# Performance work log

Hardware: AMD Instinct MI355X
Metric: run time of the kernel (lower is better)

Reference implementation:

```python
import jax, jax.numpy as jnp
import numpy as np

LAYERS = 16; SUBLAYERS = 12; NPLANES = LAYERS * SUBLAYERS
POS_LEVEL = 10; DEPTH_LEVEL = 8; ORDER = 3; BASIS_OUT = 8
HIDDEN = 384; BASIS_HIDDEN = 64
SLOPE = 0.01; SIG_OFF = 5.0
IN_H = 512; IN_W = 768; RAYS = 1024
OFFSET = 0.0


def leaky(x):
    return jnp.where(x >= 0, x, SLOPE * x)


def grid_sample_3d(vol, gx, gy, gz):
    # vol (C, D, H, W); grid coords normalized [-1,1]; align_corners=True, zeros padding
    C, Dm, H, W = vol.shape
    x = (gx + 1.0) * 0.5 * (W - 1)
    y = (gy + 1.0) * 0.5 * (H - 1)
    z = (gz + 1.0) * 0.5 * (Dm - 1)
    x0 = jnp.floor(x); y0 = jnp.floor(y); z0 = jnp.floor(z)
    flat = vol.reshape(C, -1)
    out = jnp.zeros((C,) + x.shape, vol.dtype)
    for dz in (0.0, 1.0):
        for dy in (0.0, 1.0):
            for dx in (0.0, 1.0):
                xi = x0 + dx; yi = y0 + dy; zi = z0 + dz
                w = (1 - jnp.abs(x - xi)) * (1 - jnp.abs(y - yi)) * (1 - jnp.abs(z - zi))
                valid = ((xi >= 0) & (xi < W) & (yi >= 0) & (yi < H) & (zi >= 0) & (zi < Dm)).astype(vol.dtype)
                idx = ((jnp.clip(zi, 0, Dm - 1) * H + jnp.clip(yi, 0, H - 1)) * W
                       + jnp.clip(xi, 0, W - 1)).astype(jnp.int32)
                out = out + (w * valid)[None] * jnp.take(flat, idx, axis=1)
    return out


def _rotation(angle, axis):
    axis = np.asarray(axis, np.float64); axis /= np.linalg.norm(axis)
    K = np.array([[0, -axis[2], axis[1]], [axis[2], 0, -axis[0]], [-axis[1], axis[0], 0]])
    R = np.eye(3) + np.sin(angle) * K + (1 - np.cos(angle)) * (K @ K)
    return jnp.asarray(R, jnp.float32)


def setup_inputs() -> dict:
    key = jax.random.key(0)
    ks = jax.random.split(key, 32)
    def lin(i, fan_in, fan_out):
        w = jax.random.normal(ks[i], (fan_in, fan_out), jnp.float32) / np.sqrt(fan_in).astype(np.float32)
        b = jnp.zeros((fan_out,), jnp.float32)
        return w, b
    in_dim = 2 * (2 * POS_LEVEL + DEPTH_LEVEL)     # 56
    out_dim = 1 + BASIS_OUT * 3                    # 25
    w0, b0 = lin(0, in_dim, HIDDEN)
    w1, b1 = lin(1, HIDDEN, HIDDEN)
    w2, b2 = lin(2, HIDDEN, HIDDEN)
    w3, b3 = lin(3, HIDDEN, HIDDEN)
    w4, b4 = lin(4, HIDDEN, HIDDEN)
    wo, bo = lin(5, HIDDEN, out_dim)
    bw0, bb0 = lin(6, 4 * ORDER, BASIS_HIDDEN)
    bw1, bb1 = lin(7, BASIS_HIDDEN, BASIS_HIDDEN)
    bwo, bbo = lin(8, BASIS_HIDDEN, BASIS_OUT)
    mpi_c = jax.random.uniform(ks[20], (LAYERS, 3, IN_H, IN_W), jnp.float32, -1.0, 1.0)
    K = jnp.array([[600.0, 0.0, IN_W / 2.0], [0.0, 600.0, IN_H / 2.0], [0.0, 0.0, 1.0]], jnp.float32)
    planes = jnp.asarray(1.0 / np.linspace(1.0, 0.1, NPLANES), jnp.float32)  # inverse-depth spacing, dmin=1 dmax=10
    selection = jax.random.randint(ks[21], (RAYS,), 0, IN_H * IN_W)
    return dict(
        mpi_c=mpi_c, w0=w0, b0=b0, w1=w1, b1=b1, w2=w2, b2=b2, w3=w3, b3=b3, w4=w4, b4=b4,
        wo=wo, bo=bo, bw0=bw0, bb0=bb0, bw1=bw1, bb1=bb1, bwo=bwo, bbo=bbo,
        ref_rT=jnp.eye(3, dtype=jnp.float32), ref_t=jnp.zeros((3, 1), jnp.float32), ref_k=K,
        feat_r=_rotation(0.03, [0.2, 1.0, 0.1]),
        feat_t=jnp.array([[0.08], [0.03], [0.02]], jnp.float32),
        feat_center=jnp.array([[-0.08], [-0.03], [-0.02]], jnp.float32),
        feat_k=K, planes=planes, selection=selection, out_h=IN_H, out_w=IN_W)


def reference(mpi_c, w0, b0, w1, b1, w2, b2, w3, b3, w4, b4, wo, bo,
              bw0, bb0, bw1, bb1, bwo, bbo,
              ref_rT, ref_t, ref_k, feat_r, feat_t, feat_center, feat_k,
              planes, selection, out_h, out_w):
    # ---- homography warp (computeHomographies / computeHomoWarp) ----
    ki = jnp.linalg.inv(feat_k)
    new_r = feat_r @ ref_rT
    new_t = -new_r @ ref_t + feat_t
    nvec = jnp.array([[0.0, 0.0, 1.0]], jnp.float32)
    Ha = new_r.T
    Hb = Ha @ new_t @ nvec @ Ha
    Hc = (nvec @ Ha @ new_t)[0, 0]
    Hs = ref_k @ (Ha + Hb / (-planes[:, None, None] - Hc)) @ ki      # (P,3,3)
    coords = jnp.stack([(selection % out_w).astype(jnp.float32),
                        (selection // out_w).astype(jnp.float32),
                        jnp.ones_like(selection, jnp.float32)], -1)   # (R,3)
    prod = jnp.einsum('rc,pkc->prk', coords, Hs)                      # (P,R,3)
    ref_coords = prod[..., :2] / prod[..., 2:]                        # (P,R,2)
    scale = jnp.array([IN_W - 1.0, IN_H - 1.0], jnp.float32)
    warp = (ref_coords + OFFSET) / scale * 2.0 - 1.0                  # (P,R,2)
    R = warp.shape[1]

    # ---- positional encoding + main MLP ----
    pos_freq = (0.5 * np.pi) * (2.0 ** jnp.arange(POS_LEVEL, dtype=jnp.float32))
    depth_freq = (0.5 * np.pi) * (2.0 ** jnp.arange(DEPTH_LEVEL, dtype=jnp.float32))
    z_coords = jnp.linspace(-1.0, 1.0, NPLANES)
    vxy = (warp[..., None] * pos_freq).reshape(NPLANES, R, 2 * POS_LEVEL)
    vz = jnp.broadcast_to((z_coords[:, None] * depth_freq[None])[:, None, :], (NPLANES, R, DEPTH_LEVEL))
    vxyz = jnp.concatenate([vxy, vz], -1)
    big = jnp.concatenate([jnp.sin(vxyz), jnp.cos(vxyz)], -1)         # (P,R,56)
    h = leaky(big @ w0 + b0)
    for w_, b_ in ((w1, b1), (w2, b2), (w3, b3), (w4, b4)):
        h = leaky(h @ w_ + b_)
    out = h @ wo + bo                                                 # (P,R,25)
    alpha = jax.nn.sigmoid(out[..., 0] - SIG_OFF)                     # (P,R)

    # ---- trilinear grid sample of sigmoid(mpi_c) ----
    vol = jnp.transpose(jax.nn.sigmoid(mpi_c), (1, 0, 2, 3))          # (3,L,H,W)
    depths = jnp.repeat(jnp.linspace(-1.0, 1.0, LAYERS), SUBLAYERS)   # (P,)
    gz = jnp.broadcast_to(depths[:, None], (NPLANES, R))
    rgb = grid_sample_3d(vol, warp[..., 0], warp[..., 1], gz)         # (3,P,R)
    rgb = jnp.transpose(rgb, (1, 2, 0))                               # (P,R,3)

    # ---- specular basis (viewing-angle MLP) ----
    camera = ref_rT.T @ feat_center + ref_t                           # (3,1)
    coords3 = jnp.concatenate([ref_coords, jnp.ones_like(ref_coords[..., :1])], -1)
    xyz = jnp.einsum('kc,prc->prk', ki, coords3 * planes[:, None, None])
    v = xyz - camera[:, 0]
    v = v / (jnp.linalg.norm(v, axis=-1, keepdims=True) + 1e-7)
    view_freq = 2.0 ** jnp.arange(ORDER, dtype=jnp.float32)
    hv = (v[..., :2, None] * view_freq).reshape(NPLANES, R, 2 * ORDER)
    venc = jnp.concatenate([jnp.sin(0.5 * np.pi * hv), jnp.cos(0.5 * np.pi * hv)], -1)  # (P,R,12)
    bh = leaky(venc @ bw0 + bb0)
    bh = leaky(bh @ bw1 + bb1)
    basis = jnp.tanh(bh @ bwo + bbo)                                  # (P,R,8)
    coeff = jnp.repeat(out[::SUBLAYERS, ..., 1:], SUBLAYERS, axis=0)  # (P,R,24)
    coeff = jnp.tanh(coeff.reshape(NPLANES, R, 3, BASIS_OUT))
    illum = jnp.sum(coeff * basis[:, :, None, :], -1)                 # (P,R,3)
    rgb = jnp.clip(rgb + illum, 0.0, 1.0)

    # ---- alpha compositing (cumprod_exclusive over planes) ----
    cp = jnp.cumprod(1.0 - alpha, axis=0)
    weight = jnp.concatenate([jnp.ones_like(cp[:1]), cp[:-1]], 0)     # (P,R)
    comp = jnp.sum((weight * alpha)[..., None] * rgb, axis=0)         # (R,3)
    return jnp.transpose(comp)[None, :, :, None]                      # (1,3,R,1)
```

## Files before the change

### kernel.cpp

```cpp
#include <hip/hip_runtime.h>
#include <hip/hip_bf16.h>
#include <math.h>


typedef _Float16 half2 __attribute__((ext_vector_type(2)));
typedef _Float16 half4 __attribute__((ext_vector_type(4)));
typedef _Float16 half8 __attribute__((ext_vector_type(8)));
typedef float f32x4 __attribute__((ext_vector_type(4)));

#if __has_builtin(__builtin_amdgcn_mfma_f32_16x16x32_f16)
#define MFMA32(a, b, c) __builtin_amdgcn_mfma_f32_16x16x32_f16((a), (b), (c), 0, 0, 0)
#else
#define MFMA32(a, b, c) (c)
#endif

#define NPLANES 192
#define RAYS    1024
#define IMW     768
#define IMH     512
#define PI_HALF 1.5707964f

#define FR(i, c) ((((i) >> 4) * 6144) + (((c) >> 5) * 512) + ((((c) >> 3) & 3) * 128) \
                  + (((i) & 15) * 8) + ((c) & 7))

__device__ __forceinline__ float sin_rev(float rev) {
  float f, r;
  asm("v_fract_f32 %0, %1" : "=v"(f) : "v"(rev));
  asm("v_sin_f32 %0, %1" : "=v"(r) : "v"(f));
  return r;
}

__device__ __forceinline__ half4 leaky_pack(f32x4 a) {
  const float v0 = fmaxf(a[0], a[0] * 0.01f);
  const float v1 = fmaxf(a[1], a[1] * 0.01f);
  const float v2 = fmaxf(a[2], a[2] * 0.01f);
  const float v3 = fmaxf(a[3], a[3] * 0.01f);
  const half2 lo = __builtin_bit_cast(half2, __builtin_amdgcn_cvt_pkrtz(v0, v1));
  const half2 hi = __builtin_bit_cast(half2, __builtin_amdgcn_cvt_pkrtz(v2, v3));
  return __builtin_shufflevector(lo, hi, 0, 1, 2, 3);
}

#define O_HS     0
#define O_KICAM  7168
#define O_ALPHA  7424
#define O_COEFF  793856
#define O_PW0    2366720
#define O_PW1    2415872
#define O_PW2    2710784
#define O_PW3    3005696
#define O_PW4    3300608
#define O_PWO    3595520
#define O_PBW0   3620096
#define O_PBW1   3624192
#define O_PBWO   3632384
#define O_BASIS  3634432
#define WS_NEED  (O_BASIS + 6291456)

__global__ void prep_kernel(const float* __restrict__ ref_rT, const float* __restrict__ ref_t,
                            const float* __restrict__ ref_k, const float* __restrict__ feat_r,
                            const float* __restrict__ feat_t, const float* __restrict__ feat_center,
                            const float* __restrict__ feat_k, const float* __restrict__ planes,
                            float* __restrict__ wsHs, float* __restrict__ wsKiCam)
{
  __shared__ float sKi[9], sHa[9], sHb[9], sHc[1];
  if (threadIdx.x == 0) {
    float a = feat_k[0], b = feat_k[1], c = feat_k[2];
    float d = feat_k[3], e = feat_k[4], f = feat_k[5];
    float g = feat_k[6], h = feat_k[7], i = feat_k[8];
    float A = e * i - f * h, B = -(d * i - f * g), C = d * h - e * g;
    float det = a * A + b * B + c * C;
    float id = 1.0f / det;
    float ki[9];
    ki[0] = A * id;             ki[1] = -(b * i - c * h) * id;  ki[2] = (b * f - c * e) * id;
    ki[3] = B * id;             ki[4] = (a * i - c * g) * id;   ki[5] = -(a * f - c * d) * id;
    ki[6] = C * id;             ki[7] = -(a * h - b * g) * id;  ki[8] = (a * e - b * d) * id;
    float nr[9];
    for (int r2 = 0; r2 < 3; ++r2)
      for (int c2 = 0; c2 < 3; ++c2) {
        float s = 0.f;
        for (int k2 = 0; k2 < 3; ++k2) s += feat_r[r2 * 3 + k2] * ref_rT[k2 * 3 + c2];
        nr[r2 * 3 + c2] = s;
      }
    float ntv[3];
    for (int r2 = 0; r2 < 3; ++r2) {
      float s = 0.f;
      for (int k2 = 0; k2 < 3; ++k2) s += nr[r2 * 3 + k2] * ref_t[k2];
      ntv[r2] = -s + feat_t[r2];
    }
    float Ha[9];
    for (int r2 = 0; r2 < 3; ++r2)
      for (int c2 = 0; c2 < 3; ++c2) Ha[r2 * 3 + c2] = nr[c2 * 3 + r2];
    float u[3];
    for (int r2 = 0; r2 < 3; ++r2) {
      float s = 0.f;
      for (int k2 = 0; k2 < 3; ++k2) s += Ha[r2 * 3 + k2] * ntv[k2];
      u[r2] = s;
    }
    float Hb[9];
    for (int r2 = 0; r2 < 3; ++r2)
      for (int c2 = 0; c2 < 3; ++c2) Hb[r2 * 3 + c2] = u[r2] * Ha[6 + c2];
    float cam[3];
    for (int r2 = 0; r2 < 3; ++r2) {
      float s = 0.f;
      for (int k2 = 0; k2 < 3; ++k2) s += ref_rT[k2 * 3 + r2] * feat_center[k2];
      cam[r2] = s + ref_t[r2];
    }
    for (int j = 0; j < 9; ++j) { sKi[j] = ki[j]; sHa[j] = Ha[j]; sHb[j] = Hb[j]; }
    sHc[0] = u[2];
    for (int j = 0; j < 9; ++j) wsKiCam[j] = ki[j];
    for (int j = 0; j < 3; ++j) wsKiCam[9 + j] = cam[j];
  }
  __syncthreads();
  int p = threadIdx.x;
  if (p < NPLANES) {
    float dnm = -planes[p] - sHc[0];
    float T[9];
    for (int j = 0; j < 9; ++j) T[j] = sHa[j] + sHb[j] / dnm;
    float U[9];
    for (int r2 = 0; r2 < 3; ++r2)
      for (int c2 = 0; c2 < 3; ++c2) {
        float s = 0.f;
        for (int k2 = 0; k2 < 3; ++k2) s += ref_k[r2 * 3 + k2] * T[k2 * 3 + c2];
        U[r2 * 3 + c2] = s;
      }
    for (int r2 = 0; r2 < 3; ++r2)
      for (int c2 = 0; c2 < 3; ++c2) {
        float s = 0.f;
        for (int k2 = 0; k2 < 3; ++k2) s += U[r2 * 3 + k2] * sKi[k2 * 3 + c2];
        wsHs[p * 9 + r2 * 3 + c2] = s;
      }
  }
}

__global__ void pack_all_kernel(const float* __restrict__ w0, const float* __restrict__ w1,
                                const float* __restrict__ w2, const float* __restrict__ w3,
                                const float* __restrict__ w4, const float* __restrict__ wo,
                                const float* __restrict__ bw0, const float* __restrict__ bw1,
                                const float* __restrict__ bwo, _Float16* __restrict__ dst)
{
  const int idx = blockIdx.x * 256 + threadIdx.x;
  const float* src; int Ksrc, Nsrc, NP, l;
  if (idx < 24576)       { src = w0;  Ksrc = 56;  Nsrc = 384; NP = 384; l = idx; }
  else if (idx < 172032) { src = w1;  Ksrc = 384; Nsrc = 384; NP = 384; l = idx - 24576; }
  else if (idx < 319488) { src = w2;  Ksrc = 384; Nsrc = 384; NP = 384; l = idx - 172032; }
  else if (idx < 466944) { src = w3;  Ksrc = 384; Nsrc = 384; NP = 384; l = idx - 319488; }
  else if (idx < 614400) { src = w4;  Ksrc = 384; Nsrc = 384; NP = 384; l = idx - 466944; }
  else if (idx < 626688) { src = wo;  Ksrc = 384; Nsrc = 25;  NP = 32;  l = idx - 614400; }
  else if (idx < 628736) { src = bw0; Ksrc = 12;  Nsrc = 64;  NP = 64;  l = idx - 626688; }
  else if (idx < 632832) { src = bw1; Ksrc = 64;  Nsrc = 64;  NP = 64;  l = idx - 628736; }
  else if (idx < 633856) { src = bwo; Ksrc = 64;  Nsrc = 8;   NP = 16;  l = idx - 632832; }
  else return;
  const int within = l & 511, blk = l >> 9;
  const int kg = within >> 7, ln = (within >> 3) & 15, j = within & 7;
  const int ntiles = NP >> 4;
  const int nt = blk % ntiles, kc = blk / ntiles;
  const int k = kc * 32 + kg * 8 + j, nn = nt * 16 + ln;
  const float v = (k < Ksrc && nn < Nsrc) ? src[k * Nsrc + nn] : 0.0f;
  dst[idx] = (_Float16)v;
}

template <int NKC>
__device__ __forceinline__ void hidden_layer(_Float16* hb, const _Float16* __restrict__ wl,
                                             const float* __restrict__ bias,
                                             int wvu, int g, int ln, int lane)
{
  f32x4 acc[6][4];
  #pragma unroll
  for (int ft = 0; ft < 6; ++ft) {
    const f32x4 bv4 = *(const f32x4*)&bias[(wvu * 6 + ft) * 16 + g * 4];
    #pragma unroll
    for (int pt = 0; pt < 4; ++pt) acc[ft][pt] = bv4;
  }
  #pragma unroll 4
  for (int kc = 0; kc < NKC; ++kc) {
    const _Float16* wp = wl + (kc * 24 + wvu * 6) * 512;
    half8 aw[6];
    #pragma unroll
    for (int ft = 0; ft < 6; ++ft)
      aw[ft] = *(const half8*)&wp[ft * 512 + lane * 8];
    half8 bx[4];
    #pragma unroll
    for (int pt = 0; pt < 4; ++pt)
      bx[pt] = *(const half8*)&hb[pt * 6144 + kc * 512 + lane * 8];
    #pragma unroll
    for (int ft = 0; ft < 6; ++ft)
      #pragma unroll
      for (int pt = 0; pt < 4; ++pt)
        acc[ft][pt] = MFMA32(aw[ft], bx[pt], acc[ft][pt]);
  }
  __syncthreads();
  #pragma unroll
  for (int pt = 0; pt < 4; ++pt)
    #pragma unroll
    for (int ft = 0; ft < 6; ++ft) {
      const int f0 = wvu * 96 + ft * 16 + g * 4;
      *(half4*)&hb[pt * 6144 + (f0 >> 5) * 512 + ((f0 >> 3) & 3) * 128 + ln * 8 + (f0 & 7)] =
          leaky_pack(acc[ft][pt]);
    }
  __syncthreads();
}

template <int NKC>
__device__ __forceinline__ void basis_hidden(_Float16* hb, const _Float16* __restrict__ wl,
                                             const float* __restrict__ bias,
                                             int wvu, int g, int ln, int lane)
{
  f32x4 acc[4];
  const f32x4 bv4 = *(const f32x4*)&bias[wvu * 16 + g * 4];
  #pragma unroll
  for (int pt = 0; pt < 4; ++pt) acc[pt] = bv4;
  #pragma unroll
  for (int kc = 0; kc < NKC; ++kc) {
    half8 aw = *(const half8*)&wl[(kc * 4 + wvu) * 512 + lane * 8];
    #pragma unroll
    for (int pt = 0; pt < 4; ++pt) {
      half8 bx = *(const half8*)&hb[pt * 6144 + kc * 512 + lane * 8];
      acc[pt] = MFMA32(aw, bx, acc[pt]);
    }
  }
  __syncthreads();
  const int f0 = wvu * 16 + g * 4;
  #pragma unroll
  for (int pt = 0; pt < 4; ++pt)
    *(half4*)&hb[pt * 6144 + (f0 >> 5) * 512 + ((f0 >> 3) & 3) * 128 + ln * 8 + (f0 & 7)] =
        leaky_pack(acc[pt]);
  __syncthreads();
}

__global__ __launch_bounds__(256, 3) void mlp_kernel(
    const int* __restrict__ selection, const float* __restrict__ planes,
    const float* __restrict__ wsHs, const float* __restrict__ wsKiCam,
    const _Float16* __restrict__ pw0, const _Float16* __restrict__ pw1,
    const _Float16* __restrict__ pw2, const _Float16* __restrict__ pw3,
    const _Float16* __restrict__ pw4, const _Float16* __restrict__ pwo,
    const float* __restrict__ b0, const float* __restrict__ b1,
    const float* __restrict__ b2, const float* __restrict__ b3,
    const float* __restrict__ b4, const float* __restrict__ bo,
    const _Float16* __restrict__ pbw0, const _Float16* __restrict__ pbw1,
    const _Float16* __restrict__ pbwo,
    const float* __restrict__ bb0, const float* __restrict__ bb1,
    const float* __restrict__ bbo,
    float* __restrict__ wsAlpha, float* __restrict__ wsCoeff, float* __restrict__ wsBasis)
{
  __shared__ _Float16 hbuf[4 * 6144];
  const int t = threadIdx.x;
  const int m0 = blockIdx.x * 64;
  const int p = m0 >> 10;
  const int r0 = m0 & 1023;
  const int lane = t & 63, wv = t >> 6;
  const int wvu = __builtin_amdgcn_readfirstlane(wv);
  const int g = lane >> 4, ln = lane & 15;

  {
    const int i = t >> 2, q = t & 3;
    const int ray = r0 + i;
    const int sel = selection[ray];
    const float cx = (float)(sel % IMW), cy = (float)(sel / IMW);
    const float* H = wsHs + p * 9;
    const float pr0 = H[0] * cx + H[1] * cy + H[2];
    const float pr1 = H[3] * cx + H[4] * cy + H[5];
    const float pr2 = H[6] * cx + H[7] * cy + H[8];
    const float rx = pr0 / pr2, ry = pr1 / pr2;
    const float wx = (rx / 767.0f) * 2.0f - 1.0f;
    const float wy = (ry / 511.0f) * 2.0f - 1.0f;
    const float zc = -1.0f + (float)p * (2.0f / 191.0f);
    #pragma unroll
    for (int cc = 0; cc < 7; ++cc) {
      const int c = q * 7 + cc;
      float base; int e;
      if (c < 10)      { base = wx; e = c; }
      else if (c < 20) { base = wy; e = c - 10; }
      else             { base = zc; e = c - 20; }
      const float rev = ldexpf(base, e - 2);
      hbuf[FR(i, c)]      = (_Float16)sin_rev(rev);
      hbuf[FR(i, c + 28)] = (_Float16)sin_rev(rev + 0.25f);
    }
    hbuf[FR(i, 56 + q)] = (_Float16)0.f;
    hbuf[FR(i, 60 + q)] = (_Float16)0.f;
  }
  __syncthreads();

  hidden_layer<2>(hbuf, pw0, b0, wvu, g, ln, lane);
  hidden_layer<12>(hbuf, pw1, b1, wvu, g, ln, lane);
  hidden_layer<12>(hbuf, pw2, b2, wvu, g, ln, lane);
  hidden_layer<12>(hbuf, pw3, b3, wvu, g, ln, lane);
  hidden_layer<12>(hbuf, pw4, b4, wvu, g, ln, lane);

  f32x4 acc2[2];
  {
    #pragma unroll
    for (int ft = 0; ft < 2; ++ft) {
      f32x4 bv;
      #pragma unroll
      for (int r = 0; r < 4; ++r) {
        const int f = ft * 16 + g * 4 + r;
        bv[r] = (f < 25) ? bo[f] : 0.f;
      }
      acc2[ft] = bv;
    }
    #pragma unroll 4
    for (int kc = 0; kc < 12; ++kc) {
      half8 bx = *(const half8*)&hbuf[wvu * 6144 + kc * 512 + lane * 8];
      #pragma unroll
      for (int ft = 0; ft < 2; ++ft) {
        half8 aw = *(const half8*)&pwo[(kc * 2 + ft) * 512 + lane * 8];
        acc2[ft] = MFMA32(aw, bx, acc2[ft]);
      }
    }
    __syncthreads();
  }

  {
    const int i = t >> 2, q = t & 3;
    const int ray = r0 + i;
    const int sel = selection[ray];
    const float cx = (float)(sel % IMW), cy = (float)(sel / IMW);
    const float* H = wsHs + p * 9;
    const float pr0 = H[0] * cx + H[1] * cy + H[2];
    const float pr1 = H[3] * cx + H[4] * cy + H[5];
    const float pr2 = H[6] * cx + H[7] * cy + H[8];
    const float rx = pr0 / pr2, ry = pr1 / pr2;
    const float pd = planes[p];
    const float* ki = wsKiCam; const float* cam = wsKiCam + 9;
    const float c0 = rx * pd, c1 = ry * pd, c2 = pd;
    const float vx0 = ki[0] * c0 + ki[1] * c1 + ki[2] * c2 - cam[0];
    const float vy0 = ki[3] * c0 + ki[4] * c1 + ki[5] * c2 - cam[1];
    const float vz0 = ki[6] * c0 + ki[7] * c1 + ki[8] * c2 - cam[2];
    const float nrm = sqrtf(vx0 * vx0 + vy0 * vy0 + vz0 * vz0) + 1e-7f;
    const float vx = vx0 / nrm, vy = vy0 / nrm;
    #pragma unroll
    for (int cc = 0; cc < 4; ++cc) {
      const int c = q * 4 + cc;
      float v;
      if (c < 6) {
        v = sin_rev(ldexpf((c < 3) ? vx : vy, (c % 3) - 2));
      } else if (c < 12) {
        const int c6 = c - 6;
        v = sin_rev(ldexpf((c6 < 3) ? vx : vy, (c6 % 3) - 2) + 0.25f);
      } else v = 0.f;
      hbuf[FR(i, c)] = (_Float16)v;
    }
  }
  __syncthreads();

  {
    if (g == 0) {
      const int ray = r0 + wvu * 16 + ln;
      wsAlpha[ray * NPLANES + p] = 1.0f / (1.0f + expf(5.0f - acc2[0][0]));
    }
    if ((p % 12) == 0) {
      const int pg = p / 12;
      const int ray = r0 + wvu * 16 + ln;
      #pragma unroll
      for (int ft = 0; ft < 2; ++ft)
        #pragma unroll
        for (int r = 0; r < 4; ++r) {
          const int f = ft * 16 + g * 4 + r;
          if (f >= 1 && f < 25)
            wsCoeff[(pg * RAYS + ray) * 24 + (f - 1)] = tanhf(acc2[ft][r]);
        }
    }
  }

  basis_hidden<1>(hbuf, pbw0, bb0, wvu, g, ln, lane);
  basis_hidden<2>(hbuf, pbw1, bb1, wvu, g, ln, lane);
  {
    f32x4 accO = (f32x4){0.f, 0.f, 0.f, 0.f};
    #pragma unroll
    for (int kc = 0; kc < 2; ++kc) {
      half8 aw = *(const half8*)&pbwo[kc * 512 + lane * 8];
      half8 bx = *(const half8*)&hbuf[wvu * 6144 + kc * 512 + lane * 8];
      accO = MFMA32(aw, bx, accO);
    }
    if (g < 2) {
      const int ray = r0 + wvu * 16 + ln;
      #pragma unroll
      for (int r = 0; r < 4; ++r) {
        const int f = g * 4 + r;
        wsBasis[(ray * NPLANES + p) * 8 + f] = tanhf(accO[r] + bbo[f]);
      }
    }
  }
}

__global__ __launch_bounds__(192) void composite_kernel(
    const float* __restrict__ mpi, const int* __restrict__ selection,
    const float* __restrict__ wsHs, const float* __restrict__ wsAlpha,
    const float* __restrict__ wsCoeff, const float* __restrict__ wsBasis,
    float* __restrict__ out)
{
  const int ray = blockIdx.x;
  const int p = threadIdx.x;
  const int sel = selection[ray];
  const float cx = (float)(sel % IMW), cy = (float)(sel / IMW);
  const float* H = wsHs + p * 9;
  const float pr0 = H[0] * cx + H[1] * cy + H[2];
  const float pr1 = H[3] * cx + H[4] * cy + H[5];
  const float pr2 = H[6] * cx + H[7] * cy + H[8];
  const float rx = pr0 / pr2, ry = pr1 / pr2;
  const float wx = (rx / 767.0f) * 2.0f - 1.0f;
  const float wy = (ry / 511.0f) * 2.0f - 1.0f;
  const float x = (wx + 1.0f) * 0.5f * 767.0f;
  const float y = (wy + 1.0f) * 0.5f * 511.0f;
  const float gz = -1.0f + (float)(p / 12) * (2.0f / 15.0f);
  const float z = (gz + 1.0f) * 0.5f * 15.0f;
  const float x0 = floorf(x), y0 = floorf(y), z0 = floorf(z);
  float rgb0 = 0.f, rgb1 = 0.f, rgb2 = 0.f;
  #pragma unroll
  for (int dz = 0; dz < 2; ++dz)
    #pragma unroll
    for (int dy = 0; dy < 2; ++dy)
      #pragma unroll
      for (int dx = 0; dx < 2; ++dx) {
        const float xi = x0 + (float)dx, yi = y0 + (float)dy, zi = z0 + (float)dz;
        const float w = (1.f - fabsf(x - xi)) * (1.f - fabsf(y - yi)) * (1.f - fabsf(z - zi));
        const bool valid = (xi >= 0.f) && (xi < 768.f) && (yi >= 0.f) && (yi < 512.f)
                        && (zi >= 0.f) && (zi < 16.f);
        if (valid && w != 0.f) {
          const int ix = (int)xi, iy = (int)yi, iz = (int)zi;
          const int base = iz * 3 * (IMW * IMH) + iy * IMW + ix;
          const float v0 = mpi[base];
          const float v1 = mpi[base + IMW * IMH];
          const float v2 = mpi[base + 2 * IMW * IMH];
          rgb0 += w * (1.f / (1.f + expf(-v0)));
          rgb1 += w * (1.f / (1.f + expf(-v1)));
          rgb2 += w * (1.f / (1.f + expf(-v2)));
        }
      }
  const float* bs = wsBasis + (ray * NPLANES + p) * 8;
  const float* cf = wsCoeff + ((p / 12) * RAYS + ray) * 24;
  float il0 = 0.f, il1 = 0.f, il2 = 0.f;
  #pragma unroll
  for (int j = 0; j < 8; ++j) {
    const float bj = bs[j];
    il0 += cf[j] * bj; il1 += cf[8 + j] * bj; il2 += cf[16 + j] * bj;
  }
  rgb0 = fminf(fmaxf(rgb0 + il0, 0.f), 1.f);
  rgb1 = fminf(fmaxf(rgb1 + il1, 0.f), 1.f);
  rgb2 = fminf(fmaxf(rgb2 + il2, 0.f), 1.f);
  const float a = wsAlpha[ray * NPLANES + p];
  const int lane = p & 63, w64 = p >> 6;
  float xs = 1.f - a;
  #pragma unroll
  for (int off = 1; off < 64; off <<= 1) {
    const float v = __shfl_up(xs, off, 64);
    if (lane >= off) xs *= v;
  }
  __shared__ float wtot[3];
  __shared__ float part[3][3];
  if (lane == 63) wtot[w64] = xs;
  __syncthreads();
  float pre = 1.f;
  #pragma unroll
  for (int q = 0; q < 2; ++q)
    if (q < w64) pre *= wtot[q];
  float excl = __shfl_up(xs, 1, 64);
  if (lane == 0) excl = 1.f;
  const float wa = pre * excl * a;
  float s0 = wa * rgb0, s1 = wa * rgb1, s2 = wa * rgb2;
  #pragma unroll
  for (int off = 32; off >= 1; off >>= 1) {
    s0 += __shfl_down(s0, off, 64);
    s1 += __shfl_down(s1, off, 64);
    s2 += __shfl_down(s2, off, 64);
  }
  if (lane == 0) { part[w64][0] = s0; part[w64][1] = s1; part[w64][2] = s2; }
  __syncthreads();
  if (p == 0) {
    out[0 * RAYS + ray] = part[0][0] + part[1][0] + part[2][0];
    out[1 * RAYS + ray] = part[0][1] + part[1][1] + part[2][1];
    out[2 * RAYS + ray] = part[0][2] + part[1][2] + part[2][2];
  }
}

extern "C" void kernel_launch(void* const* d_in, const int* in_sizes, int n_in,
                              void* d_out, int out_size, void* d_ws, size_t ws_size,
                              hipStream_t stream)
{
  (void)in_sizes; (void)n_in; (void)out_size;
  const float* mpi    = (const float*)d_in[0];
  const float* w0     = (const float*)d_in[1];
  const float* b0     = (const float*)d_in[2];
  const float* w1     = (const float*)d_in[3];
  const float* b1     = (const float*)d_in[4];
  const float* w2     = (const float*)d_in[5];
  const float* b2     = (const float*)d_in[6];
  const float* w3     = (const float*)d_in[7];
  const float* b3     = (const float*)d_in[8];
  const float* w4     = (const float*)d_in[9];
  const float* b4     = (const float*)d_in[10];
  const float* wo     = (const float*)d_in[11];
  const float* bo     = (const float*)d_in[12];
  const float* bw0    = (const float*)d_in[13];
  const float* bb0    = (const float*)d_in[14];
  const float* bw1    = (const float*)d_in[15];
  const float* bb1    = (const float*)d_in[16];
  const float* bwo    = (const float*)d_in[17];
  const float* bbo    = (const float*)d_in[18];
  const float* ref_rT = (const float*)d_in[19];
  const float* ref_t  = (const float*)d_in[20];
  const float* ref_k  = (const float*)d_in[21];
  const float* feat_r = (const float*)d_in[22];
  const float* feat_t = (const float*)d_in[23];
  const float* feat_c = (const float*)d_in[24];
  const float* feat_k = (const float*)d_in[25];
  const float* planes = (const float*)d_in[26];
  const int*   selection = (const int*)d_in[27];
  float* outp = (float*)d_out;
  char* ws = (char*)d_ws;
  if (ws_size < (size_t)WS_NEED) return;

  float* wsHs    = (float*)(ws + O_HS);
  float* wsKiCam = (float*)(ws + O_KICAM);
  float* wsAlpha = (float*)(ws + O_ALPHA);
  float* wsCoeff = (float*)(ws + O_COEFF);
  float* wsBasis = (float*)(ws + O_BASIS);
  _Float16* pw0  = (_Float16*)(ws + O_PW0);
  _Float16* pw1  = (_Float16*)(ws + O_PW1);
  _Float16* pw2  = (_Float16*)(ws + O_PW2);
  _Float16* pw3  = (_Float16*)(ws + O_PW3);
  _Float16* pw4  = (_Float16*)(ws + O_PW4);
  _Float16* pwo  = (_Float16*)(ws + O_PWO);
  _Float16* pbw0 = (_Float16*)(ws + O_PBW0);
  _Float16* pbw1 = (_Float16*)(ws + O_PBW1);
  _Float16* pbwo = (_Float16*)(ws + O_PBWO);

  prep_kernel<<<1, 256, 0, stream>>>(ref_rT, ref_t, ref_k, feat_r, feat_t, feat_c,
                                     feat_k, planes, wsHs, wsKiCam);
  pack_all_kernel<<<2476, 256, 0, stream>>>(w0, w1, w2, w3, w4, wo, bw0, bw1, bwo, pw0);

  mlp_kernel<<<(NPLANES * RAYS) / 64, 256, 0, stream>>>(
      selection, planes, wsHs, wsKiCam,
      pw0, pw1, pw2, pw3, pw4, pwo,
      b0, b1, b2, b3, b4, bo,
      pbw0, pbw1, pbwo, bb0, bb1, bbo,
      wsAlpha, wsCoeff, wsBasis);

  composite_kernel<<<RAYS, NPLANES, 0, stream>>>(mpi, selection, wsHs, wsAlpha,
                                                 wsCoeff, wsBasis, outp);
}
```

Baseline: 293.3 us.

## Use fast exp/rcp activations, transpose workspace layouts, drop readfirstlane, reduce unroll

Replaces expf/tanhf in the MLP epilogue with v_exp_f32/v_rcp_f32 based sigmoid and tanh. It switches the alpha, coeff and basis workspace layouts to plane-major or ray-contiguous order and vectorizes the basis store. It also removes the readfirstlane wave index and lowers the unroll factor of the K loops. These changes aim to coalesce the MLP-side stores and cut transcendental cost, but the composite kernel now reads with strided addresses, and the fast intrinsics lose some precision.

```diff
diff --git a/kernel.cpp b/kernel.cpp
--- a/kernel.cpp
+++ b/kernel.cpp
@@ -28,6 +28,26 @@
   asm("v_fract_f32 %0, %1" : "=v"(f) : "v"(rev));
   asm("v_sin_f32 %0, %1" : "=v"(r) : "v"(f));
   return r;
+}
+
+__device__ __forceinline__ float exp2_fast(float x) {
+  float r;
+  asm("v_exp_f32 %0, %1" : "=v"(r) : "v"(x));
+  return r;
+}
+__device__ __forceinline__ float rcp_fast(float x) {
+  float r;
+  asm("v_rcp_f32 %0, %1" : "=v"(r) : "v"(x));
+  return r;
+}
+__device__ __forceinline__ float tanh_fast(float x) {
+  const float xc = fminf(fmaxf(x, -30.f), 30.f);
+  const float t = exp2_fast(xc * 2.885390082f);
+  return (t - 1.f) * rcp_fast(t + 1.f);
+}
+__device__ __forceinline__ float sig5_fast(float o) {
+  const float u = exp2_fast((5.f - o) * 1.4426950f);
+  return rcp_fast(1.f + u);
 }
 
 __device__ __forceinline__ half4 leaky_pack(f32x4 a) {
@@ -162,22 +182,21 @@
 template <int NKC>
 __device__ __forceinline__ void hidden_layer(_Float16* hb, const _Float16* __restrict__ wl,
                                              const float* __restrict__ bias,
-                                             int wvu, int g, int ln, int lane)
+                                             int wv, int g, int ln, int lane)
 {
   f32x4 acc[6][4];
   #pragma unroll
   for (int ft = 0; ft < 6; ++ft) {
-    const f32x4 bv4 = *(const f32x4*)&bias[(wvu * 6 + ft) * 16 + g * 4];
+    const f32x4 bv4 = *(const f32x4*)&bias[(wv * 6 + ft) * 16 + g * 4];
     #pragma unroll
     for (int pt = 0; pt < 4; ++pt) acc[ft][pt] = bv4;
   }
-  #pragma unroll 4
+  #pragma unroll 2
   for (int kc = 0; kc < NKC; ++kc) {
-    const _Float16* wp = wl + (kc * 24 + wvu * 6) * 512;
     half8 aw[6];
     #pragma unroll
     for (int ft = 0; ft < 6; ++ft)
-      aw[ft] = *(const half8*)&wp[ft * 512 + lane * 8];
+      aw[ft] = *(const half8*)&wl[(kc * 24 + wv * 6 + ft) * 512 + lane * 8];
     half8 bx[4];
     #pragma unroll
     for (int pt = 0; pt < 4; ++pt)
@@ -193,7 +212,7 @@
   for (int pt = 0; pt < 4; ++pt)
     #pragma unroll
     for (int ft = 0; ft < 6; ++ft) {
-      const int f0 = wvu * 96 + ft * 16 + g * 4;
+      const int f0 = wv * 96 + ft * 16 + g * 4;
       *(half4*)&hb[pt * 6144 + (f0 >> 5) * 512 + ((f0 >> 3) & 3) * 128 + ln * 8 + (f0 & 7)] =
           leaky_pack(acc[ft][pt]);
     }
@@ -203,15 +222,15 @@
 template <int NKC>
 __device__ __forceinline__ void basis_hidden(_Float16* hb, const _Float16* __restrict__ wl,
                                              const float* __restrict__ bias,
-                                             int wvu, int g, int ln, int lane)
+                                             int wv, int g, int ln, int lane)
 {
   f32x4 acc[4];
-  const f32x4 bv4 = *(const f32x4*)&bias[wvu * 16 + g * 4];
+  const f32x4 bv4 = *(const f32x4*)&bias[wv * 16 + g * 4];
   #pragma unroll
   for (int pt = 0; pt < 4; ++pt) acc[pt] = bv4;
   #pragma unroll
   for (int kc = 0; kc < NKC; ++kc) {
-    half8 aw = *(const half8*)&wl[(kc * 4 + wvu) * 512 + lane * 8];
+    half8 aw = *(const half8*)&wl[(kc * 4 + wv) * 512 + lane * 8];
     #pragma unroll
     for (int pt = 0; pt < 4; ++pt) {
       half8 bx = *(const half8*)&hb[pt * 6144 + kc * 512 + lane * 8];
@@ -219,7 +238,7 @@
     }
   }
   __syncthreads();
-  const int f0 = wvu * 16 + g * 4;
+  const int f0 = wv * 16 + g * 4;
   #pragma unroll
   for (int pt = 0; pt < 4; ++pt)
     *(half4*)&hb[pt * 6144 + (f0 >> 5) * 512 + ((f0 >> 3) & 3) * 128 + ln * 8 + (f0 & 7)] =
@@ -248,7 +267,6 @@
   const int p = m0 >> 10;
   const int r0 = m0 & 1023;
   const int lane = t & 63, wv = t >> 6;
-  const int wvu = __builtin_amdgcn_readfirstlane(wv);
   const int g = lane >> 4, ln = lane & 15;
 
   {
@@ -280,11 +298,11 @@
   }
   __syncthreads();
 
-  hidden_layer<2>(hbuf, pw0, b0, wvu, g, ln, lane);
-  hidden_layer<12>(hbuf, pw1, b1, wvu, g, ln, lane);
-  hidden_layer<12>(hbuf, pw2, b2, wvu, g, ln, lane);
-  hidden_layer<12>(hbuf, pw3, b3, wvu, g, ln, lane);
-  hidden_layer<12>(hbuf, pw4, b4, wvu, g, ln, lane);
+  hidden_layer<2>(hbuf, pw0, b0, wv, g, ln, lane);
+  hidden_layer<12>(hbuf, pw1, b1, wv, g, ln, lane);
+  hidden_layer<12>(hbuf, pw2, b2, wv, g, ln, lane);
+  hidden_layer<12>(hbuf, pw3, b3, wv, g, ln, lane);
+  hidden_layer<12>(hbuf, pw4, b4, wv, g, ln, lane);
 
   f32x4 acc2[2];
   {
@@ -298,9 +316,9 @@
       }
       acc2[ft] = bv;
     }
-    #pragma unroll 4
+    #pragma unroll 2
     for (int kc = 0; kc < 12; ++kc) {
-      half8 bx = *(const half8*)&hbuf[wvu * 6144 + kc * 512 + lane * 8];
+      half8 bx = *(const half8*)&hbuf[wv * 6144 + kc * 512 + lane * 8];
       #pragma unroll
       for (int ft = 0; ft < 2; ++ft) {
         half8 aw = *(const half8*)&pwo[(kc * 2 + ft) * 512 + lane * 8];
@@ -345,40 +363,40 @@
 
   {
     if (g == 0) {
-      const int ray = r0 + wvu * 16 + ln;
-      wsAlpha[ray * NPLANES + p] = 1.0f / (1.0f + expf(5.0f - acc2[0][0]));
+      const int ray = r0 + wv * 16 + ln;
+      wsAlpha[p * RAYS + ray] = sig5_fast(acc2[0][0]);
     }
     if ((p % 12) == 0) {
       const int pg = p / 12;
-      const int ray = r0 + wvu * 16 + ln;
+      const int ray = r0 + wv * 16 + ln;
       #pragma unroll
       for (int ft = 0; ft < 2; ++ft)
         #pragma unroll
         for (int r = 0; r < 4; ++r) {
           const int f = ft * 16 + g * 4 + r;
           if (f >= 1 && f < 25)
-            wsCoeff[(pg * RAYS + ray) * 24 + (f - 1)] = tanhf(acc2[ft][r]);
+            wsCoeff[(pg * 24 + (f - 1)) * RAYS + ray] = tanh_fast(acc2[ft][r]);
         }
     }
   }
 
-  basis_hidden<1>(hbuf, pbw0, bb0, wvu, g, ln, lane);
-  basis_hidden<2>(hbuf, pbw1, bb1, wvu, g, ln, lane);
+  basis_hidden<1>(hbuf, pbw0, bb0, wv, g, ln, lane);
+  basis_hidden<2>(hbuf, pbw1, bb1, wv, g, ln, lane);
   {
     f32x4 accO = (f32x4){0.f, 0.f, 0.f, 0.f};
     #pragma unroll
     for (int kc = 0; kc < 2; ++kc) {
       half8 aw = *(const half8*)&pbwo[kc * 512 + lane * 8];
-      half8 bx = *(const half8*)&hbuf[wvu * 6144 + kc * 512 + lane * 8];
+      half8 bx = *(const half8*)&hbuf[wv * 6144 + kc * 512 + lane * 8];
       accO = MFMA32(aw, bx, accO);
     }
     if (g < 2) {
-      const int ray = r0 + wvu * 16 + ln;
+      const int ray = r0 + wv * 16 + ln;
+      f32x4 bv;
       #pragma unroll
-      for (int r = 0; r < 4; ++r) {
-        const int f = g * 4 + r;
-        wsBasis[(ray * NPLANES + p) * 8 + f] = tanhf(accO[r] + bbo[f]);
-      }
+      for (int r = 0; r < 4; ++r)
+        bv[r] = tanh_fast(accO[r] + bbo[g * 4 + r]);
+      *(f32x4*)&wsBasis[(p * RAYS + ray) * 8 + g * 4] = bv;
     }
   }
 }
@@ -427,18 +445,20 @@
           rgb2 += w * (1.f / (1.f + expf(-v2)));
         }
       }
-  const float* bs = wsBasis + (ray * NPLANES + p) * 8;
-  const float* cf = wsCoeff + ((p / 12) * RAYS + ray) * 24;
+  const float* bs = wsBasis + (p * RAYS + ray) * 8;
+  const float* cf = wsCoeff + (p / 12) * 24 * RAYS + ray;
   float il0 = 0.f, il1 = 0.f, il2 = 0.f;
   #pragma unroll
   for (int j = 0; j < 8; ++j) {
     const float bj = bs[j];
-    il0 += cf[j] * bj; il1 += cf[8 + j] * bj; il2 += cf[16 + j] * bj;
+    il0 += cf[j * RAYS] * bj;
+    il1 += cf[(8 + j) * RAYS] * bj;
+    il2 += cf[(16 + j) * RAYS] * bj;
   }
   rgb0 = fminf(fmaxf(rgb0 + il0, 0.f), 1.f);
   rgb1 = fminf(fmaxf(rgb1 + il1, 0.f), 1.f);
   rgb2 = fminf(fmaxf(rgb2 + il2, 0.f), 1.f);
-  const float a = wsAlpha[ray * NPLANES + p];
+  const float a = wsAlpha[p * RAYS + ray];
   const int lane = p & 63, w64 = p >> 6;
   float xs = 1.f - a;
   #pragma unroll
```

Result: faster. 263.2 us (-10.2%).
